# Kernel optimization log

Measured on AMD Instinct MI355X. Metric: run time of the kernel, lower is better.

## Reference

```python
import jax, jax.numpy as jnp
import numpy as np

N_PTS0 = 32   # sample points per line
N_PTS1 = 8    # after 1d max-pool (kernel 4)
DIM_LOI = 128
DIM_FC = 1024
TOPK = 300
H = W = 128
L = 10000
C_FEAT = 256


def setup_inputs() -> dict:
    key = jax.random.key(0)
    ks = jax.random.split(key, 8)
    f32 = jnp.float32
    return {
        'output': jax.random.normal(ks[0], (1, 9, H, W), f32),
        'features': jax.random.normal(ks[1], (1, C_FEAT, H, W), f32),
        'lines_pred': jax.random.uniform(ks[2], (L, 4), f32, 0.0, W - 1.0),
        'fc1_w': jax.random.normal(ks[3], (DIM_LOI, C_FEAT), f32) * 0.05,
        'fc1_b': jnp.zeros((DIM_LOI,), f32),
        'w1': jax.random.normal(ks[4], (DIM_FC, DIM_LOI * N_PTS1), f32) * 0.02,
        'b1': jnp.zeros((DIM_FC,), f32),
        'w2': jax.random.normal(ks[5], (DIM_FC, DIM_FC), f32) * 0.02,
        'b2': jnp.zeros((DIM_FC,), f32),
        'w3': jax.random.normal(ks[6], (1, DIM_FC), f32) * 0.02,
        'b3': jnp.zeros((1,), f32),
    }


def _nms(a):
    # a: [H, W]; 3x3 max-pool NMS, keep only local maxima
    ap = jax.lax.reduce_window(a[None, None], -jnp.inf, jax.lax.max,
                               (1, 1, 3, 3), (1, 1, 1, 1), 'SAME')[0, 0]
    return a * (a == ap).astype(a.dtype)


def _pooling(loi, lines, w1, b1, w2, b2, w3, b3):
    # loi: [D, H, W]; lines: [L, 4]
    h, w = loi.shape[1], loi.shape[2]
    tspan = jnp.linspace(0.0, 1.0, N_PTS0)[None, None, :]          # [1,1,P]
    U, V = lines[:, :2], lines[:, 2:]
    pts = U[:, :, None] * tspan + V[:, :, None] * (1.0 - tspan) - 0.5  # [L,2,P]
    pts = jnp.transpose(pts, (0, 2, 1)).reshape(-1, 2)              # [L*P,2]
    px, py = pts[:, 0], pts[:, 1]
    px0 = jnp.clip(jnp.floor(px), 0, w - 1)
    py0 = jnp.clip(jnp.floor(py), 0, h - 1)
    px1 = jnp.clip(px0 + 1, 0, w - 1)
    py1 = jnp.clip(py0 + 1, 0, h - 1)
    ix0, iy0 = px0.astype(jnp.int32), py0.astype(jnp.int32)
    ix1, iy1 = px1.astype(jnp.int32), py1.astype(jnp.int32)
    xp = (loi[:, iy0, ix0] * (py1 - py) * (px1 - px)
          + loi[:, iy1, ix0] * (py - py0) * (px1 - px)
          + loi[:, iy0, ix1] * (py1 - py) * (px - px0)
          + loi[:, iy1, ix1] * (py - py0) * (px - px0))              # [D, L*P]
    xp = jnp.transpose(xp.reshape(DIM_LOI, -1, N_PTS0), (1, 0, 2))  # [L,D,P]
    k = N_PTS0 // N_PTS1
    xp = xp.reshape(xp.shape[0], DIM_LOI, N_PTS1, k).max(-1)        # maxpool1d
    feat = xp.reshape(-1, DIM_LOI * N_PTS1)                         # [L, D*P1]
    hid = jax.nn.relu(feat @ w1.T + b1)
    hid = jax.nn.relu(hid @ w2.T + b2)
    return (hid @ w3.T + b3).ravel()                                # logits [L]


def reference(output, features, lines_pred, fc1_w, fc1_b, w1, b1, w2, b2, w3, b3):
    height, width = output.shape[2], output.shape[3]
    # head decode
    jloc = jax.nn.softmax(output[0, 5:7], axis=0)[1]      # [H,W]
    joff = jax.nn.sigmoid(output[0, 7:9]) - 0.5           # [2,H,W]
    # NMS + top-k junction extraction
    jflat = _nms(jloc).reshape(-1)
    jscores, index = jax.lax.top_k(jflat, TOPK)
    joff_f = joff.reshape(2, -1)
    y = (index // width).astype(jnp.float32) + joff_f[1, index] + 0.5
    x = (index % width).astype(jnp.float32) + joff_f[0, index] + 0.5
    juncs = jnp.stack((x, y), axis=1)                     # [K,2]
    # pairwise endpoint-to-junction matching
    d1 = jnp.sum((lines_pred[None, :, :2] - juncs[:, None]) ** 2, -1)  # [K,L]
    d2 = jnp.sum((lines_pred[None, :, 2:] - juncs[:, None]) ** 2, -1)
    idx1 = jnp.argmin(d1, axis=0)
    idx2 = jnp.argmin(d2, axis=0)
    imin = jnp.minimum(idx1, idx2)
    imax = jnp.maximum(idx1, idx2)
    keep = imin < imax                                    # degenerate-line mask
    lines_adj = jnp.concatenate((juncs[imin], juncs[imax]), axis=1)  # [L,4]
    # 1x1 conv LOI features + bilinear line sampling + MLP verification
    loi = jnp.einsum('chw,dc->dhw', features[0], fc1_w) + fc1_b[:, None, None]
    logits = _pooling(loi, lines_adj, w1, b1, w2, b2, w3, b3)
    line_scores = jax.nn.sigmoid(logits) * keep.astype(logits.dtype)
    return line_scores, lines_adj, juncs, jscores
```

## Files before the change

kernel.cpp:

```cpp
#include <hip/hip_runtime.h>
#include <stdint.h>

#define HW      16384
#define WIDTH   128
#define NTOPK   300
#define NLINES  10000
#define MPAD2   10240

typedef unsigned short u16;
typedef unsigned int   u32;
typedef unsigned long long u64;
typedef __bf16 bf16x8 __attribute__((ext_vector_type(8)));
typedef float  f32x4  __attribute__((ext_vector_type(4)));

__device__ __forceinline__ u16 f2bf(float f) {
  u32 x = __builtin_bit_cast(u32, f);
  x += 0x7FFFu + ((x >> 16) & 1u);
  return (u16)(x >> 16);
}
__device__ __forceinline__ float bf2f(u32 u) {
  return __builtin_bit_cast(float, u << 16);
}
__device__ __forceinline__ void gload_lds16(void* lds, const void* g) {
  __builtin_amdgcn_global_load_lds(
      (const __attribute__((address_space(1))) void*)g,
      (__attribute__((address_space(3))) void*)lds, 16, 0, 0);
}

#define CF asm volatile("" ::: "memory")
#define BAR do { CF; __builtin_amdgcn_s_barrier(); CF; } while (0)
#define VM4 asm volatile("s_waitcnt vmcnt(4)" ::: "memory")
#define VM0 asm volatile("s_waitcnt vmcnt(0)" ::: "memory")

__global__ __launch_bounds__(256) void k_nms(const float* __restrict__ out9,
                                             float* __restrict__ jnms) {
  __shared__ float jl[18][18];
  int t = threadIdx.x;
  int gx0 = blockIdx.x * 16 - 1, gy0 = blockIdx.y * 16 - 1;
  for (int lin = t; lin < 324; lin += 256) {
    int lx = lin % 18, ly = lin / 18;
    int gx = gx0 + lx, gy = gy0 + ly;
    float v = -__builtin_inff();
    if (gx >= 0 && gx < WIDTH && gy >= 0 && gy < WIDTH) {
      int i = gy * WIDTH + gx;
      v = 1.f / (1.f + expf(out9[5 * HW + i] - out9[6 * HW + i]));
    }
    jl[ly][lx] = v;
  }
  __syncthreads();
  int tx = t & 15, ty = t >> 4;
  float a = jl[ty + 1][tx + 1], m = a;
#pragma unroll
  for (int dy = 0; dy < 3; ++dy)
#pragma unroll
    for (int dx = 0; dx < 3; ++dx)
      m = fmaxf(m, jl[ty + dy][tx + dx]);
  int gx = blockIdx.x * 16 + tx, gy = blockIdx.y * 16 + ty;
  jnms[gy * WIDTH + gx] = (a == m) ? a : 0.f;
}

__global__ __launch_bounds__(1024) void k_topk(const float* __restrict__ jnms,
                                               const float* __restrict__ out9,
                                               float* __restrict__ juncs_ws,
                                               float* __restrict__ out_juncs,
                                               float* __restrict__ out_jsc) {
  __shared__ u64 keys[4096];
  __shared__ int cnt;
  int t = threadIdx.x;
  if (t == 0) cnt = 0;
  __syncthreads();
  for (int i = t; i < HW; i += 1024) {
    float v = jnms[i];
    if (v > 0.f) {
      int pos = atomicAdd(&cnt, 1);
      if (pos < 4096)
        keys[pos] = ((u64)__builtin_bit_cast(u32, v) << 32) | (u32)(0xFFFFFFFFu - (u32)i);
    }
  }
  __syncthreads();
  int c = cnt < 4096 ? cnt : 4096;
  int n = (c <= 2048) ? 2048 : 4096;
  for (int i = t; i < n; i += 1024)
    if (i >= c) keys[i] = 0ull;
  __syncthreads();
  for (int k = 2; k <= n; k <<= 1) {
    for (int j = k >> 1; j > 0; j >>= 1) {
      for (int u = t; u < (n >> 1); u += 1024) {
        int i  = ((u & ~(j - 1)) << 1) | (u & (j - 1));
        int p  = i | j;
        u64 a = keys[i], b = keys[p];
        bool dir = (i & k) == 0;
        if ((a < b) == dir) { keys[i] = b; keys[p] = a; }
      }
      __syncthreads();
    }
  }
  if (t < NTOPK) {
    u64 key = keys[t];
    u32 vb  = (u32)(key >> 32);
    int idx = (int)(0xFFFFFFFFu - (u32)(key & 0xFFFFFFFFu));
    float ox = 1.f / (1.f + expf(-out9[7 * HW + idx])) - 0.5f;
    float oy = 1.f / (1.f + expf(-out9[8 * HW + idx])) - 0.5f;
    float x = (float)(idx & (WIDTH - 1)) + ox + 0.5f;
    float y = (float)(idx >> 7)          + oy + 0.5f;
    juncs_ws[2 * t] = x; juncs_ws[2 * t + 1] = y;
    out_juncs[2 * t] = x; out_juncs[2 * t + 1] = y;
    out_jsc[t] = __builtin_bit_cast(float, vb);
  }
}

__global__ __launch_bounds__(256) void k_match(const float* __restrict__ juncs,
                                               const float* __restrict__ lines_pred,
                                               float* __restrict__ lines_adj,
                                               float* __restrict__ keepf) {
  __shared__ float jl[2 * NTOPK];
  int t = threadIdx.x;
  for (int i = t; i < 2 * NTOPK; i += 256) jl[i] = juncs[i];
  __syncthreads();
  int wid = t >> 6, lane = t & 63;
  int l = blockIdx.x * 4 + wid;
  if (l >= NLINES) return;
  float lx1 = lines_pred[l * 4 + 0], ly1 = lines_pred[l * 4 + 1];
  float lx2 = lines_pred[l * 4 + 2], ly2 = lines_pred[l * 4 + 3];
  float b1 = __builtin_inff(), b2 = __builtin_inff();
  int i1 = 0, i2 = 0;
  for (int j = lane; j < NTOPK; j += 64) {
    float jx = jl[2 * j], jy = jl[2 * j + 1];
    float dx = __fsub_rn(lx1, jx), dy = __fsub_rn(ly1, jy);
    float d  = __fadd_rn(__fmul_rn(dx, dx), __fmul_rn(dy, dy));
    if (d < b1) { b1 = d; i1 = j; }
    dx = __fsub_rn(lx2, jx); dy = __fsub_rn(ly2, jy);
    d  = __fadd_rn(__fmul_rn(dx, dx), __fmul_rn(dy, dy));
    if (d < b2) { b2 = d; i2 = j; }
  }
#pragma unroll
  for (int off = 1; off < 64; off <<= 1) {
    float d_o = __shfl_xor(b1, off, 64); int i_o = __shfl_xor(i1, off, 64);
    if (d_o < b1 || (d_o == b1 && i_o < i1)) { b1 = d_o; i1 = i_o; }
    d_o = __shfl_xor(b2, off, 64); i_o = __shfl_xor(i2, off, 64);
    if (d_o < b2 || (d_o == b2 && i_o < i2)) { b2 = d_o; i2 = i_o; }
  }
  if (lane == 0) {
    int imin = i1 < i2 ? i1 : i2;
    int imax = i1 < i2 ? i2 : i1;
    lines_adj[l * 4 + 0] = jl[2 * imin];
    lines_adj[l * 4 + 1] = jl[2 * imin + 1];
    lines_adj[l * 4 + 2] = jl[2 * imax];
    lines_adj[l * 4 + 3] = jl[2 * imax + 1];
    keepf[l] = (imin < imax) ? 1.f : 0.f;
  }
}

__global__ __launch_bounds__(256) void k_transp(const float* __restrict__ features,
                                                u16* __restrict__ featT) {
  __shared__ float tile[64][65];
  int t = threadIdx.x;
  int p0 = blockIdx.x * 64, c0 = blockIdx.y * 64;
#pragma unroll
  for (int i = 0; i < 4; ++i) {
    int lin = i * 256 + t;
    int c = lin >> 4, p4 = (lin & 15) * 4;
    float4 v = *(const float4*)&features[(size_t)(c0 + c) * HW + p0 + p4];
    tile[c][p4 + 0] = v.x; tile[c][p4 + 1] = v.y;
    tile[c][p4 + 2] = v.z; tile[c][p4 + 3] = v.w;
  }
  __syncthreads();
#pragma unroll
  for (int i = 0; i < 2; ++i) {
    int lin = i * 256 + t;
    int p = lin >> 3, c8 = (lin & 7) * 8;
    uint4 pk;
    pk.x = (u32)f2bf(tile[c8 + 0][p]) | ((u32)f2bf(tile[c8 + 1][p]) << 16);
    pk.y = (u32)f2bf(tile[c8 + 2][p]) | ((u32)f2bf(tile[c8 + 3][p]) << 16);
    pk.z = (u32)f2bf(tile[c8 + 4][p]) | ((u32)f2bf(tile[c8 + 5][p]) << 16);
    pk.w = (u32)f2bf(tile[c8 + 6][p]) | ((u32)f2bf(tile[c8 + 7][p]) << 16);
    *(uint4*)&featT[(size_t)(p0 + p) * 256 + c0 + c8] = pk;
  }
}

__device__ __forceinline__ void acc8(uint4 r, float wg, float* a) {
  a[0] += bf2f(r.x & 0xffffu) * wg; a[1] += bf2f(r.x >> 16) * wg;
  a[2] += bf2f(r.y & 0xffffu) * wg; a[3] += bf2f(r.y >> 16) * wg;
  a[4] += bf2f(r.z & 0xffffu) * wg; a[5] += bf2f(r.z >> 16) * wg;
  a[6] += bf2f(r.w & 0xffffu) * wg; a[7] += bf2f(r.w >> 16) * wg;
}
__global__ __launch_bounds__(256) void k_interp(const u16* __restrict__ loib,
                                                const float* __restrict__ lines_adj,
                                                u16* __restrict__ feat) {
  __shared__ u16 outb[8][128];
  int l = blockIdx.x;
  int t = threadIdx.x;
  int w = t >> 6, lane = t & 63;
  int q = lane >> 4, chgrp = lane & 15;
  float ux = lines_adj[l * 4 + 0], uy = lines_adj[l * 4 + 1];
  float vx = lines_adj[l * 4 + 2], vy = lines_adj[l * 4 + 3];
#pragma unroll
  for (int it = 0; it < 2; ++it) {
    int s = it * 4 + w;
    int p = s * 4 + q;
    float tt = (float)p / 31.f;
    float px = ux * tt + vx * (1.f - tt) - 0.5f;
    float py = uy * tt + vy * (1.f - tt) - 0.5f;
    float px0 = fminf(fmaxf(floorf(px), 0.f), 127.f);
    float py0 = fminf(fmaxf(floorf(py), 0.f), 127.f);
    float px1 = fminf(px0 + 1.f, 127.f);
    float py1 = fminf(py0 + 1.f, 127.f);
    int ix0 = (int)px0, iy0 = (int)py0, ix1 = (int)px1, iy1 = (int)py1;
    float wy1 = py1 - py, wy0 = py - py0, wx1 = px1 - px, wx0 = px - px0;
    int co = chgrp * 8;
    uint4 v00 = *(const uint4*)&loib[(iy0 * WIDTH + ix0) * 128 + co];
    uint4 v10 = *(const uint4*)&loib[(iy1 * WIDTH + ix0) * 128 + co];
    uint4 v01 = *(const uint4*)&loib[(iy0 * WIDTH + ix1) * 128 + co];
    uint4 v11 = *(const uint4*)&loib[(iy1 * WIDTH + ix1) * 128 + co];
    float a[8];
#pragma unroll
    for (int c = 0; c < 8; ++c) a[c] = 0.f;
    acc8(v00, wy1 * wx1, a);
    acc8(v10, wy0 * wx1, a);
    acc8(v01, wy1 * wx0, a);
    acc8(v11, wy0 * wx0, a);
#pragma unroll
    for (int c = 0; c < 8; ++c) {
      float v = fmaxf(a[c], __shfl_xor(a[c], 16, 64));
      v = fmaxf(v, __shfl_xor(v, 32, 64));
      a[c] = v;
    }
    if (q == 0) {
      uint4 pk;
      pk.x = (u32)f2bf(a[0]) | ((u32)f2bf(a[1]) << 16);
      pk.y = (u32)f2bf(a[2]) | ((u32)f2bf(a[3]) << 16);
      pk.z = (u32)f2bf(a[4]) | ((u32)f2bf(a[5]) << 16);
      pk.w = (u32)f2bf(a[6]) | ((u32)f2bf(a[7]) << 16);
      *(uint4*)&outb[s][co] = pk;
    }
  }
  __syncthreads();
  int ch = t >> 1, s0 = (t & 1) * 4;
  u16 e0 = outb[s0 + 0][ch], e1 = outb[s0 + 1][ch];
  u16 e2 = outb[s0 + 2][ch], e3 = outb[s0 + 3][ch];
  uint2 pk;
  pk.x = (u32)e0 | ((u32)e1 << 16);
  pk.y = (u32)e2 | ((u32)e3 << 16);
  *(uint2*)&feat[(size_t)l * 1024 + ch * 8 + s0] = pk;
}

__global__ __launch_bounds__(256) void k_cvt(const float* __restrict__ src,
                                             u16* __restrict__ dst, int n) {
  int i = (blockIdx.x * 256 + threadIdx.x) * 4;
  if (i >= n) return;
  float4 v = *(const float4*)&src[i];
  uint2 pk;
  pk.x = (u32)f2bf(v.x) | ((u32)f2bf(v.y) << 16);
  pk.y = (u32)f2bf(v.z) | ((u32)f2bf(v.w) << 16);
  *(uint2*)&dst[i] = pk;
}

template <int RELU>
__global__ __launch_bounds__(256) void k_gemm128(const u16* __restrict__ A,
                                                 const u16* __restrict__ B,
                                                 const float* __restrict__ bias,
                                                 u16* __restrict__ C,
                                                 int M, int N, int K) {
  __shared__ u16 Alds[128 * 32];
  __shared__ u16 Blds[128 * 32];
  int nwg = gridDim.x * gridDim.y;
  int bid = blockIdx.y * gridDim.x + blockIdx.x;
  int cpx = nwg >> 3;
  int key = (bid & 7) * cpx + (bid >> 3);
  int bx = key / gridDim.y;
  int by = key % gridDim.y;
  int t = threadIdx.x;
  int tm0 = bx * 128;
  int tn0 = by * 128;
  int lane = t & 63, wid = t >> 6;
  int wr = wid >> 1, wc = wid & 1;
  f32x4 acc[4][4] = {};
  int arow = t >> 2, apos = (t & 3) * 8;
  const u16* Abase = A + (size_t)tm0 * K;
  const u16* Bbase = B + (size_t)tn0 * K;
  int r = lane & 15, ks = (lane >> 4) * 8;
  for (int k0 = 0; k0 < K; k0 += 32) {
    gload_lds16(&Alds[(size_t)t * 8],         Abase + (size_t)arow * K + k0 + apos);
    gload_lds16(&Alds[(size_t)(t + 256) * 8], Abase + (size_t)(arow + 64) * K + k0 + apos);
    gload_lds16(&Blds[(size_t)t * 8],         Bbase + (size_t)arow * K + k0 + apos);
    gload_lds16(&Blds[(size_t)(t + 256) * 8], Bbase + (size_t)(arow + 64) * K + k0 + apos);
    __syncthreads();
    bf16x8 af[4], bfr[4];
#pragma unroll
    for (int i = 0; i < 4; ++i) {
      af[i]  = *(const bf16x8*)&Alds[(wr * 64 + i * 16 + r) * 32 + ks];
      bfr[i] = *(const bf16x8*)&Blds[(wc * 64 + i * 16 + r) * 32 + ks];
    }
#pragma unroll
    for (int mi = 0; mi < 4; ++mi)
#pragma unroll
      for (int ni = 0; ni < 4; ++ni)
        acc[mi][ni] = __builtin_amdgcn_mfma_f32_16x16x32_bf16(af[mi], bfr[ni], acc[mi][ni], 0, 0, 0);
    __syncthreads();
  }
  int rsub = (lane >> 4) * 4, csub = lane & 15;
#pragma unroll
  for (int mi = 0; mi < 4; ++mi) {
#pragma unroll
    for (int ni = 0; ni < 4; ++ni) {
      int col = tn0 + wc * 64 + ni * 16 + csub;
      float bv = bias[col];
#pragma unroll
      for (int j = 0; j < 4; ++j) {
        int row = tm0 + wr * 64 + mi * 16 + rsub + j;
        float v = acc[mi][ni][j] + bv;
        if (RELU) v = fmaxf(v, 0.f);
        C[(size_t)row * N + col] = f2bf(v);
      }
    }
  }
}

__device__ __forceinline__ void stg256(u16* S, int ldsbase, const u16* Xb,
                                       size_t sbase, int K, int kt, int h, int dbase) {
  gload_lds16(&S[ldsbase + h * 8192 + dbase],
              Xb + sbase + (size_t)(h * 128) * K + kt * 64);
  gload_lds16(&S[ldsbase + h * 8192 + 4096 + dbase],
              Xb + sbase + (size_t)(h * 128 + 64) * K + kt * 64);
}
template <int RH>
__device__ __forceinline__ void lda4(bf16x8 (*dst)[2], const u16* Sa, int rowA,
                                     int kx0, int kx1) {
#pragma unroll
  for (int f = 0; f < 4; ++f) {
    const u16* p = Sa + rowA + (RH * 64 + f * 16) * 64;
    dst[f][0] = *(const bf16x8*)&p[kx0];
    dst[f][1] = *(const bf16x8*)&p[kx1];
  }
}
template <int CH>
__device__ __forceinline__ void ldb2(bf16x8 (*dst)[2], const u16* Sb, int rowB,
                                     int kx0, int kx1) {
#pragma unroll
  for (int cf = 0; cf < 2; ++cf) {
    const u16* p = Sb + rowB + (CH * 32 + cf * 16) * 64;
    dst[cf][0] = *(const bf16x8*)&p[kx0];
    dst[cf][1] = *(const bf16x8*)&p[kx1];
  }
}
template <int RH, int CH>
__device__ __forceinline__ void mm16(f32x4 (*acc)[4], bf16x8 (*af)[2], bf16x8 (*bf)[2]) {
  __builtin_amdgcn_s_setprio(1);
#pragma unroll
  for (int f = 0; f < 4; ++f)
#pragma unroll
    for (int cf = 0; cf < 2; ++cf) {
      f32x4 a = acc[RH * 4 + f][CH * 2 + cf];
      a = __builtin_amdgcn_mfma_f32_16x16x32_bf16(af[f][0], bf[cf][0], a, 0, 0, 0);
      a = __builtin_amdgcn_mfma_f32_16x16x32_bf16(af[f][1], bf[cf][1], a, 0, 0, 0);
      acc[RH * 4 + f][CH * 2 + cf] = a;
    }
  __builtin_amdgcn_s_setprio(0);
}

template <int RELU, int HEAD>
__global__ __launch_bounds__(512, 2) void k_gemm256(const u16* __restrict__ A,
                                                    const u16* __restrict__ B,
                                                    const float* __restrict__ bias,
                                                    u16* __restrict__ C,
                                                    const float* __restrict__ w3,
                                                    float* __restrict__ partial,
                                                    int M, int N, int K) {
  __shared__ u16 S[65536];
  const int t = threadIdx.x, lane = t & 63, w = t >> 6;
  const int wm = w >> 2, wn = w & 3;
  int nwg = gridDim.x * gridDim.y;
  int bid = blockIdx.y * gridDim.x + blockIdx.x;
  int cpx = nwg >> 3;
  int key = (bid & 7) * cpx + (bid >> 3);
  int bx = key / gridDim.y, by = key % gridDim.y;
  const u16* Ab = A + (size_t)(bx * 256) * K;
  const u16* Bb = B + (size_t)(by * 256) * K;
  const int srow = w * 8 + (lane >> 3);
  const size_t sbase = (size_t)srow * K + ((lane & 7) ^ (lane >> 3)) * 8;
  const int dbase = w * 512 + lane * 8;
  const int l15 = lane & 15, hi = lane >> 4, l7 = lane & 7;
  const int rowA = (wm * 128 + l15) * 64;
  const int rowB = (wn * 64 + l15) * 64;
  const int kx0 = ((0 + hi) ^ l7) * 8;
  const int kx1 = ((4 + hi) ^ l7) * 8;
  const u16* SA0 = S;
  const u16* SA1 = S + 16384;
  const u16* SB0 = S + 32768;
  const u16* SB1 = S + 49152;
  f32x4 acc[8][4] = {};
  bf16x8 af0[4][2], af1[4][2], bf0[2][2], bf1[2][2];
  const int NI = K >> 7;
  stg256(S, 0,     Ab, sbase, K, 0, 0, dbase);
  stg256(S, 0,     Ab, sbase, K, 0, 1, dbase);
  stg256(S, 32768, Bb, sbase, K, 0, 0, dbase);
  stg256(S, 32768, Bb, sbase, K, 0, 1, dbase);
  stg256(S, 16384, Ab, sbase, K, 1, 0, dbase);
  stg256(S, 16384, Ab, sbase, K, 1, 1, dbase);
  VM4; BAR;
  for (int j = 0; j < NI - 1; ++j) {
    int kt = 2 * j;
    lda4<0>(af0, SA0, rowA, kx0, kx1);
    ldb2<0>(bf0, SB0, rowB, kx0, kx1);
    stg256(S, 49152, Bb, sbase, K, kt + 1, 0, dbase);
    BAR; mm16<0, 0>(acc, af0, bf0); BAR;
    lda4<1>(af1, SA0, rowA, kx0, kx1);
    stg256(S, 49152, Bb, sbase, K, kt + 1, 1, dbase);
    BAR; mm16<1, 0>(acc, af1, bf0); BAR;
    ldb2<1>(bf1, SB0, rowB, kx0, kx1);
    stg256(S, 0, Ab, sbase, K, kt + 2, 0, dbase);
    BAR; mm16<0, 1>(acc, af0, bf1); BAR;
    stg256(S, 0, Ab, sbase, K, kt + 2, 1, dbase);
    VM4;
    BAR; mm16<1, 1>(acc, af1, bf1); BAR;
    lda4<0>(af0, SA1, rowA, kx0, kx1);
    ldb2<0>(bf0, SB1, rowB, kx0, kx1);
    stg256(S, 32768, Bb, sbase, K, kt + 2, 0, dbase);
    BAR; mm16<0, 0>(acc, af0, bf0); BAR;
    lda4<1>(af1, SA1, rowA, kx0, kx1);
    stg256(S, 32768, Bb, sbase, K, kt + 2, 1, dbase);
    BAR; mm16<1, 0>(acc, af1, bf0); BAR;
    ldb2<1>(bf1, SB1, rowB, kx0, kx1);
    stg256(S, 16384, Ab, sbase, K, kt + 3, 0, dbase);
    BAR; mm16<0, 1>(acc, af0, bf1); BAR;
    stg256(S, 16384, Ab, sbase, K, kt + 3, 1, dbase);
    VM4;
    BAR; mm16<1, 1>(acc, af1, bf1); BAR;
  }
  {
    int kt = 2 * (NI - 1);
    lda4<0>(af0, SA0, rowA, kx0, kx1);
    ldb2<0>(bf0, SB0, rowB, kx0, kx1);
    stg256(S, 49152, Bb, sbase, K, kt + 1, 0, dbase);
    BAR; mm16<0, 0>(acc, af0, bf0); BAR;
    lda4<1>(af1, SA0, rowA, kx0, kx1);
    stg256(S, 49152, Bb, sbase, K, kt + 1, 1, dbase);
    BAR; mm16<1, 0>(acc, af1, bf0); BAR;
    ldb2<1>(bf1, SB0, rowB, kx0, kx1);
    BAR; mm16<0, 1>(acc, af0, bf1); BAR;
    VM0;
    BAR; mm16<1, 1>(acc, af1, bf1); BAR;
    lda4<0>(af0, SA1, rowA, kx0, kx1);
    ldb2<0>(bf0, SB1, rowB, kx0, kx1);
    BAR; mm16<0, 0>(acc, af0, bf0); BAR;
    lda4<1>(af1, SA1, rowA, kx0, kx1);
    BAR; mm16<1, 0>(acc, af1, bf0); BAR;
    ldb2<1>(bf1, SB1, rowB, kx0, kx1);
    BAR; mm16<0, 1>(acc, af0, bf1); BAR;
    mm16<1, 1>(acc, af1, bf1);
  }
  int row0 = bx * 256 + wm * 128 + hi * 4;
  int col0 = by * 256 + wn * 64 + l15;
  if (HEAD == 0) {
#pragma unroll
    for (int f = 0; f < 8; ++f) {
#pragma unroll
      for (int cf = 0; cf < 4; ++cf) {
        float bv = bias[col0 + cf * 16];
#pragma unroll
        for (int jj = 0; jj < 4; ++jj) {
          float v = acc[f][cf][jj] + bv;
          if (RELU) v = fmaxf(v, 0.f);
          C[(size_t)(row0 + f * 16 + jj) * N + col0 + cf * 16] = f2bf(v);
        }
      }
    }
  } else {
    float bv[4], wv[4];
#pragma unroll
    for (int cf = 0; cf < 4; ++cf) {
      bv[cf] = bias[col0 + cf * 16];
      wv[cf] = w3[col0 + cf * 16];
    }
#pragma unroll
    for (int f = 0; f < 8; ++f) {
#pragma unroll
      for (int jj = 0; jj < 4; ++jj) {
        float p = 0.f;
#pragma unroll
        for (int cf = 0; cf < 4; ++cf) {
          float v = acc[f][cf][jj] + bv[cf];
          v = fmaxf(v, 0.f);
          p += v * wv[cf];
        }
        p += __shfl_xor(p, 1, 64);
        p += __shfl_xor(p, 2, 64);
        p += __shfl_xor(p, 4, 64);
        p += __shfl_xor(p, 8, 64);
        if (l15 == 0)
          partial[(size_t)(by * 4 + wn) * M + row0 + f * 16 + jj] = p;
      }
    }
  }
}

__global__ __launch_bounds__(256) void k_head2(const float* __restrict__ partial,
                                               const float* __restrict__ b3,
                                               const float* __restrict__ keepf,
                                               float* __restrict__ scores, int M) {
  int l = blockIdx.x * 256 + threadIdx.x;
  if (l >= NLINES) return;
  float s = 0.f;
#pragma unroll
  for (int i = 0; i < 16; ++i) s += partial[(size_t)i * M + l];
  float logit = s + b3[0];
  scores[l] = keepf[l] / (1.f + expf(-logit));
}

extern "C" void kernel_launch(void* const* d_in, const int* in_sizes, int n_in,
                              void* d_out, int out_size, void* d_ws, size_t ws_size,
                              hipStream_t stream) {
  const float* t_output   = (const float*)d_in[0];
  const float* t_features = (const float*)d_in[1];
  const float* t_lines    = (const float*)d_in[2];
  const float* t_fc1w     = (const float*)d_in[3];
  const float* t_fc1b     = (const float*)d_in[4];
  const float* t_w1       = (const float*)d_in[5];
  const float* t_b1       = (const float*)d_in[6];
  const float* t_w2       = (const float*)d_in[7];
  const float* t_b2       = (const float*)d_in[8];
  const float* t_w3       = (const float*)d_in[9];
  const float* t_b3       = (const float*)d_in[10];

  char* w = (char*)d_ws;
  u16*   loib  = (u16*)w;
  float* jnms  = (float*)(w + 4194304);
  float* juncs = jnms + HW;
  float* keepf = juncs + 1024;
  u16* fc1wb = (u16*)(keepf + 10240);
  u16* w1b  = fc1wb + 32768;
  u16* w2b  = w1b + 1048576;
  u16* feat = w2b + 1048576;
  u16* hid1 = feat + (size_t)MPAD2 * 1024;
  float* partial = (float*)(hid1 + (size_t)MPAD2 * 1024);
  u16* featT = hid1;

  float* out_scores = (float*)d_out;
  float* out_ladj   = out_scores + NLINES;
  float* out_juncs  = out_scores + 50000;
  float* out_jsc    = out_scores + 50600;

  k_nms<<<dim3(8, 8), 256, 0, stream>>>(t_output, jnms);
  k_topk<<<1, 1024, 0, stream>>>(jnms, t_output, juncs, out_juncs, out_jsc);
  k_match<<<2500, 256, 0, stream>>>(juncs, t_lines, out_ladj, keepf);
  k_cvt<<<32, 256, 0, stream>>>(t_fc1w, fc1wb, 32768);
  k_transp<<<dim3(256, 4), 256, 0, stream>>>(t_features, featT);
  k_gemm128<0><<<dim3(128, 1), 256, 0, stream>>>(featT, fc1wb, t_fc1b, loib, HW, 128, 256);
  k_interp<<<NLINES, 256, 0, stream>>>(loib, out_ladj, feat);
  k_cvt<<<1024, 256, 0, stream>>>(t_w1, w1b, 1048576);
  k_cvt<<<1024, 256, 0, stream>>>(t_w2, w2b, 1048576);
  k_gemm256<1, 0><<<dim3(40, 4), 512, 0, stream>>>(feat, w1b, t_b1, hid1,
                                                   nullptr, nullptr, MPAD2, 1024, 1024);
  k_gemm256<0, 1><<<dim3(40, 4), 512, 0, stream>>>(hid1, w2b, t_b2, nullptr,
                                                   t_w3, partial, MPAD2, 1024, 1024);
  k_head2<<<40, 256, 0, stream>>>(partial, t_b3, keepf, out_scores, MPAD2);
}
```

Before: 167.9 us.

## Fuse NMS into top-k, match into interpolation, and merge weight conversions

Junction NMS now runs inside the single-block top-k kernel through an LDS sigmoid map. Line-to-junction matching is fused with bilinear sampling, so each wave interpolates its own line without a round trip through global memory. The three fp32-to-bf16 weight conversions become one launch. This removes four kernel launches and one intermediate buffer. The cost is that the single-block top-k kernel now also computes the 16K sigmoids and the NMS serially, and interpolation runs on 4 lines per block instead of 1 line per block.

```diff
diff --git a/kernel.cpp b/kernel.cpp
--- a/kernel.cpp
+++ b/kernel.cpp
@@ -32,49 +32,34 @@
 #define VM4 asm volatile("s_waitcnt vmcnt(4)" ::: "memory")
 #define VM0 asm volatile("s_waitcnt vmcnt(0)" ::: "memory")
 
-__global__ __launch_bounds__(256) void k_nms(const float* __restrict__ out9,
-                                             float* __restrict__ jnms) {
-  __shared__ float jl[18][18];
-  int t = threadIdx.x;
-  int gx0 = blockIdx.x * 16 - 1, gy0 = blockIdx.y * 16 - 1;
-  for (int lin = t; lin < 324; lin += 256) {
-    int lx = lin % 18, ly = lin / 18;
-    int gx = gx0 + lx, gy = gy0 + ly;
-    float v = -__builtin_inff();
-    if (gx >= 0 && gx < WIDTH && gy >= 0 && gy < WIDTH) {
-      int i = gy * WIDTH + gx;
-      v = 1.f / (1.f + expf(out9[5 * HW + i] - out9[6 * HW + i]));
-    }
-    jl[ly][lx] = v;
-  }
-  __syncthreads();
-  int tx = t & 15, ty = t >> 4;
-  float a = jl[ty + 1][tx + 1], m = a;
-#pragma unroll
-  for (int dy = 0; dy < 3; ++dy)
-#pragma unroll
-    for (int dx = 0; dx < 3; ++dx)
-      m = fmaxf(m, jl[ty + dy][tx + dx]);
-  int gx = blockIdx.x * 16 + tx, gy = blockIdx.y * 16 + ty;
-  jnms[gy * WIDTH + gx] = (a == m) ? a : 0.f;
-}
-
-__global__ __launch_bounds__(1024) void k_topk(const float* __restrict__ jnms,
-                                               const float* __restrict__ out9,
+__global__ __launch_bounds__(1024) void k_topk(const float* __restrict__ out9,
                                                float* __restrict__ juncs_ws,
                                                float* __restrict__ out_juncs,
                                                float* __restrict__ out_jsc) {
+  __shared__ float sig[HW];
   __shared__ u64 keys[4096];
   __shared__ int cnt;
   int t = threadIdx.x;
   if (t == 0) cnt = 0;
+  for (int i = t; i < HW; i += 1024)
+    sig[i] = 1.f / (1.f + expf(out9[5 * HW + i] - out9[6 * HW + i]));
   __syncthreads();
   for (int i = t; i < HW; i += 1024) {
-    float v = jnms[i];
-    if (v > 0.f) {
+    int x = i & (WIDTH - 1), y = i >> 7;
+    float a = sig[i], m = a;
+    for (int dy = -1; dy <= 1; ++dy) {
+      int yy = y + dy;
+      if (yy < 0 || yy >= WIDTH) continue;
+      for (int dx = -1; dx <= 1; ++dx) {
+        int xx = x + dx;
+        if (xx < 0 || xx >= WIDTH) continue;
+        m = fmaxf(m, sig[yy * WIDTH + xx]);
+      }
+    }
+    if (a == m) {
       int pos = atomicAdd(&cnt, 1);
       if (pos < 4096)
-        keys[pos] = ((u64)__builtin_bit_cast(u32, v) << 32) | (u32)(0xFFFFFFFFu - (u32)i);
+        keys[pos] = ((u64)__builtin_bit_cast(u32, a) << 32) | (u32)(0xFFFFFFFFu - (u32)i);
     }
   }
   __syncthreads();
@@ -109,17 +94,25 @@
   }
 }
 
-__global__ __launch_bounds__(256) void k_match(const float* __restrict__ juncs,
-                                               const float* __restrict__ lines_pred,
-                                               float* __restrict__ lines_adj,
-                                               float* __restrict__ keepf) {
+__device__ __forceinline__ void acc8(uint4 r, float wg, float* a) {
+  a[0] += bf2f(r.x & 0xffffu) * wg; a[1] += bf2f(r.x >> 16) * wg;
+  a[2] += bf2f(r.y & 0xffffu) * wg; a[3] += bf2f(r.y >> 16) * wg;
+  a[4] += bf2f(r.z & 0xffffu) * wg; a[5] += bf2f(r.z >> 16) * wg;
+  a[6] += bf2f(r.w & 0xffffu) * wg; a[7] += bf2f(r.w >> 16) * wg;
+}
+__global__ __launch_bounds__(256) void k_minterp(const float* __restrict__ juncs,
+                                                 const float* __restrict__ lines_pred,
+                                                 const u16* __restrict__ loib,
+                                                 float* __restrict__ lines_adj,
+                                                 float* __restrict__ keepf,
+                                                 u16* __restrict__ feat) {
   __shared__ float jl[2 * NTOPK];
+  __shared__ u16 outb[4][8][128];
   int t = threadIdx.x;
   for (int i = t; i < 2 * NTOPK; i += 256) jl[i] = juncs[i];
   __syncthreads();
-  int wid = t >> 6, lane = t & 63;
-  int l = blockIdx.x * 4 + wid;
-  if (l >= NLINES) return;
+  int w = t >> 6, lane = t & 63;
+  int l = blockIdx.x * 4 + w;
   float lx1 = lines_pred[l * 4 + 0], ly1 = lines_pred[l * 4 + 1];
   float lx2 = lines_pred[l * 4 + 2], ly2 = lines_pred[l * 4 + 3];
   float b1 = __builtin_inff(), b2 = __builtin_inff();
@@ -140,63 +133,20 @@
     d_o = __shfl_xor(b2, off, 64); i_o = __shfl_xor(i2, off, 64);
     if (d_o < b2 || (d_o == b2 && i_o < i2)) { b2 = d_o; i2 = i_o; }
   }
+  int imin = i1 < i2 ? i1 : i2;
+  int imax = i1 < i2 ? i2 : i1;
+  float ux = jl[2 * imin], uy = jl[2 * imin + 1];
+  float vx = jl[2 * imax], vy = jl[2 * imax + 1];
   if (lane == 0) {
-    int imin = i1 < i2 ? i1 : i2;
-    int imax = i1 < i2 ? i2 : i1;
-    lines_adj[l * 4 + 0] = jl[2 * imin];
-    lines_adj[l * 4 + 1] = jl[2 * imin + 1];
-    lines_adj[l * 4 + 2] = jl[2 * imax];
-    lines_adj[l * 4 + 3] = jl[2 * imax + 1];
+    lines_adj[l * 4 + 0] = ux;
+    lines_adj[l * 4 + 1] = uy;
+    lines_adj[l * 4 + 2] = vx;
+    lines_adj[l * 4 + 3] = vy;
     keepf[l] = (imin < imax) ? 1.f : 0.f;
   }
-}
-
-__global__ __launch_bounds__(256) void k_transp(const float* __restrict__ features,
-                                                u16* __restrict__ featT) {
-  __shared__ float tile[64][65];
-  int t = threadIdx.x;
-  int p0 = blockIdx.x * 64, c0 = blockIdx.y * 64;
-#pragma unroll
-  for (int i = 0; i < 4; ++i) {
-    int lin = i * 256 + t;
-    int c = lin >> 4, p4 = (lin & 15) * 4;
-    float4 v = *(const float4*)&features[(size_t)(c0 + c) * HW + p0 + p4];
-    tile[c][p4 + 0] = v.x; tile[c][p4 + 1] = v.y;
-    tile[c][p4 + 2] = v.z; tile[c][p4 + 3] = v.w;
-  }
-  __syncthreads();
-#pragma unroll
-  for (int i = 0; i < 2; ++i) {
-    int lin = i * 256 + t;
-    int p = lin >> 3, c8 = (lin & 7) * 8;
-    uint4 pk;
-    pk.x = (u32)f2bf(tile[c8 + 0][p]) | ((u32)f2bf(tile[c8 + 1][p]) << 16);
-    pk.y = (u32)f2bf(tile[c8 + 2][p]) | ((u32)f2bf(tile[c8 + 3][p]) << 16);
-    pk.z = (u32)f2bf(tile[c8 + 4][p]) | ((u32)f2bf(tile[c8 + 5][p]) << 16);
-    pk.w = (u32)f2bf(tile[c8 + 6][p]) | ((u32)f2bf(tile[c8 + 7][p]) << 16);
-    *(uint4*)&featT[(size_t)(p0 + p) * 256 + c0 + c8] = pk;
-  }
-}
-
-__device__ __forceinline__ void acc8(uint4 r, float wg, float* a) {
-  a[0] += bf2f(r.x & 0xffffu) * wg; a[1] += bf2f(r.x >> 16) * wg;
-  a[2] += bf2f(r.y & 0xffffu) * wg; a[3] += bf2f(r.y >> 16) * wg;
-  a[4] += bf2f(r.z & 0xffffu) * wg; a[5] += bf2f(r.z >> 16) * wg;
-  a[6] += bf2f(r.w & 0xffffu) * wg; a[7] += bf2f(r.w >> 16) * wg;
-}
-__global__ __launch_bounds__(256) void k_interp(const u16* __restrict__ loib,
-                                                const float* __restrict__ lines_adj,
-                                                u16* __restrict__ feat) {
-  __shared__ u16 outb[8][128];
-  int l = blockIdx.x;
-  int t = threadIdx.x;
-  int w = t >> 6, lane = t & 63;
-  int q = lane >> 4, chgrp = lane & 15;
-  float ux = lines_adj[l * 4 + 0], uy = lines_adj[l * 4 + 1];
-  float vx = lines_adj[l * 4 + 2], vy = lines_adj[l * 4 + 3];
-#pragma unroll
-  for (int it = 0; it < 2; ++it) {
-    int s = it * 4 + w;
+  int q = lane >> 4, chgrp = lane & 15, co = chgrp * 8;
+#pragma unroll
+  for (int s = 0; s < 8; ++s) {
     int p = s * 4 + q;
     float tt = (float)p / 31.f;
     float px = ux * tt + vx * (1.f - tt) - 0.5f;
@@ -207,23 +157,22 @@
     float py1 = fminf(py0 + 1.f, 127.f);
     int ix0 = (int)px0, iy0 = (int)py0, ix1 = (int)px1, iy1 = (int)py1;
     float wy1 = py1 - py, wy0 = py - py0, wx1 = px1 - px, wx0 = px - px0;
-    int co = chgrp * 8;
     uint4 v00 = *(const uint4*)&loib[(iy0 * WIDTH + ix0) * 128 + co];
     uint4 v10 = *(const uint4*)&loib[(iy1 * WIDTH + ix0) * 128 + co];
     uint4 v01 = *(const uint4*)&loib[(iy0 * WIDTH + ix1) * 128 + co];
     uint4 v11 = *(const uint4*)&loib[(iy1 * WIDTH + ix1) * 128 + co];
     float a[8];
 #pragma unroll
-    for (int c = 0; c < 8; ++c) a[c] = 0.f;
+    for (int cc = 0; cc < 8; ++cc) a[cc] = 0.f;
     acc8(v00, wy1 * wx1, a);
     acc8(v10, wy0 * wx1, a);
     acc8(v01, wy1 * wx0, a);
     acc8(v11, wy0 * wx0, a);
 #pragma unroll
-    for (int c = 0; c < 8; ++c) {
-      float v = fmaxf(a[c], __shfl_xor(a[c], 16, 64));
+    for (int cc = 0; cc < 8; ++cc) {
+      float v = fmaxf(a[cc], __shfl_xor(a[cc], 16, 64));
       v = fmaxf(v, __shfl_xor(v, 32, 64));
-      a[c] = v;
+      a[cc] = v;
     }
     if (q == 0) {
       uint4 pk;
@@ -231,28 +180,66 @@
       pk.y = (u32)f2bf(a[2]) | ((u32)f2bf(a[3]) << 16);
       pk.z = (u32)f2bf(a[4]) | ((u32)f2bf(a[5]) << 16);
       pk.w = (u32)f2bf(a[6]) | ((u32)f2bf(a[7]) << 16);
-      *(uint4*)&outb[s][co] = pk;
+      *(uint4*)&outb[w][s][co] = pk;
     }
   }
   __syncthreads();
-  int ch = t >> 1, s0 = (t & 1) * 4;
-  u16 e0 = outb[s0 + 0][ch], e1 = outb[s0 + 1][ch];
-  u16 e2 = outb[s0 + 2][ch], e3 = outb[s0 + 3][ch];
-  uint2 pk;
-  pk.x = (u32)e0 | ((u32)e1 << 16);
-  pk.y = (u32)e2 | ((u32)e3 << 16);
-  *(uint2*)&feat[(size_t)l * 1024 + ch * 8 + s0] = pk;
-}
-
-__global__ __launch_bounds__(256) void k_cvt(const float* __restrict__ src,
-                                             u16* __restrict__ dst, int n) {
-  int i = (blockIdx.x * 256 + threadIdx.x) * 4;
-  if (i >= n) return;
-  float4 v = *(const float4*)&src[i];
+#pragma unroll
+  for (int cc = 0; cc < 2; ++cc) {
+    int ch = lane * 2 + cc;
+    uint4 pk;
+    pk.x = (u32)outb[w][0][ch] | ((u32)outb[w][1][ch] << 16);
+    pk.y = (u32)outb[w][2][ch] | ((u32)outb[w][3][ch] << 16);
+    pk.z = (u32)outb[w][4][ch] | ((u32)outb[w][5][ch] << 16);
+    pk.w = (u32)outb[w][6][ch] | ((u32)outb[w][7][ch] << 16);
+    *(uint4*)&feat[(size_t)l * 1024 + ch * 8] = pk;
+  }
+}
+
+__global__ __launch_bounds__(256) void k_transp(const float* __restrict__ features,
+                                                u16* __restrict__ featT) {
+  __shared__ float tile[64][65];
+  int t = threadIdx.x;
+  int p0 = blockIdx.x * 64, c0 = blockIdx.y * 64;
+#pragma unroll
+  for (int i = 0; i < 4; ++i) {
+    int lin = i * 256 + t;
+    int c = lin >> 4, p4 = (lin & 15) * 4;
+    float4 v = *(const float4*)&features[(size_t)(c0 + c) * HW + p0 + p4];
+    tile[c][p4 + 0] = v.x; tile[c][p4 + 1] = v.y;
+    tile[c][p4 + 2] = v.z; tile[c][p4 + 3] = v.w;
+  }
+  __syncthreads();
+#pragma unroll
+  for (int i = 0; i < 2; ++i) {
+    int lin = i * 256 + t;
+    int p = lin >> 3, c8 = (lin & 7) * 8;
+    uint4 pk;
+    pk.x = (u32)f2bf(tile[c8 + 0][p]) | ((u32)f2bf(tile[c8 + 1][p]) << 16);
+    pk.y = (u32)f2bf(tile[c8 + 2][p]) | ((u32)f2bf(tile[c8 + 3][p]) << 16);
+    pk.z = (u32)f2bf(tile[c8 + 4][p]) | ((u32)f2bf(tile[c8 + 5][p]) << 16);
+    pk.w = (u32)f2bf(tile[c8 + 6][p]) | ((u32)f2bf(tile[c8 + 7][p]) << 16);
+    *(uint4*)&featT[(size_t)(p0 + p) * 256 + c0 + c8] = pk;
+  }
+}
+
+__global__ __launch_bounds__(256) void k_cvt3(const float* __restrict__ w1,
+                                              const float* __restrict__ w2,
+                                              const float* __restrict__ fc1,
+                                              u16* __restrict__ d1,
+                                              u16* __restrict__ d2,
+                                              u16* __restrict__ d3) {
+  int b = blockIdx.x;
+  const float* s; u16* d; int base;
+  if (b < 1024)      { s = w1;  d = d1; base = b * 1024; }
+  else if (b < 2048) { s = w2;  d = d2; base = (b - 1024) * 1024; }
+  else               { s = fc1; d = d3; base = (b - 2048) * 1024; }
+  int i = base + threadIdx.x * 4;
+  float4 v = *(const float4*)&s[i];
   uint2 pk;
   pk.x = (u32)f2bf(v.x) | ((u32)f2bf(v.y) << 16);
   pk.y = (u32)f2bf(v.z) | ((u32)f2bf(v.w) << 16);
-  *(uint2*)&dst[i] = pk;
+  *(uint2*)&d[i] = pk;
 }
 
 template <int RELU>
@@ -524,8 +511,7 @@
 
   char* w = (char*)d_ws;
   u16*   loib  = (u16*)w;
-  float* jnms  = (float*)(w + 4194304);
-  float* juncs = jnms + HW;
+  float* juncs = (float*)(w + 4194304);
   float* keepf = juncs + 1024;
   u16* fc1wb = (u16*)(keepf + 10240);
   u16* w1b  = fc1wb + 32768;
@@ -540,15 +526,11 @@
   float* out_juncs  = out_scores + 50000;
   float* out_jsc    = out_scores + 50600;
 
-  k_nms<<<dim3(8, 8), 256, 0, stream>>>(t_output, jnms);
-  k_topk<<<1, 1024, 0, stream>>>(jnms, t_output, juncs, out_juncs, out_jsc);
-  k_match<<<2500, 256, 0, stream>>>(juncs, t_lines, out_ladj, keepf);
-  k_cvt<<<32, 256, 0, stream>>>(t_fc1w, fc1wb, 32768);
+  k_cvt3<<<2080, 256, 0, stream>>>(t_w1, t_w2, t_fc1w, w1b, w2b, fc1wb);
+  k_topk<<<1, 1024, 0, stream>>>(t_output, juncs, out_juncs, out_jsc);
   k_transp<<<dim3(256, 4), 256, 0, stream>>>(t_features, featT);
   k_gemm128<0><<<dim3(128, 1), 256, 0, stream>>>(featT, fc1wb, t_fc1b, loib, HW, 128, 256);
-  k_interp<<<NLINES, 256, 0, stream>>>(loib, out_ladj, feat);
-  k_cvt<<<1024, 256, 0, stream>>>(t_w1, w1b, 1048576);
-  k_cvt<<<1024, 256, 0, stream>>>(t_w2, w2b, 1048576);
+  k_minterp<<<2500, 256, 0, stream>>>(juncs, t_lines, loib, out_ladj, keepf, feat);
   k_gemm256<1, 0><<<dim3(40, 4), 512, 0, stream>>>(feat, w1b, t_b1, hid1,
                                                    nullptr, nullptr, MPAD2, 1024, 1024);
   k_gemm256<0, 1><<<dim3(40, 4), 512, 0, stream>>>(hid1, w2b, t_b2, nullptr,
```

After: 165.1 us. About the same (-1.7%).
